# Optimization experiments

Hardware: AMD Instinct MI355X
Metric: run time of the kernel (lower is better)

## Reference

```python
import jax, jax.numpy as jnp
import numpy as np

H = W = 128      # image_shape
B = 64           # batch_size
O = 32           # orbit_size
RADIANS = True   # args.radians
RADIAN_INIT = 1.57
AFFINE_INIT = 0.1


def setup_inputs() -> dict:
    key = jax.random.key(0)
    k1, k2 = jax.random.split(key)
    X = jax.random.normal(k1, (B, H * W), dtype=jnp.float32)
    eps = jax.random.uniform(k2, (O, 7), dtype=jnp.float32)
    base = np.array([3.14, 1.0, 1.0, 1.0, 1.0, 1.0, 1.0], np.float32)
    ident = np.array([RADIAN_INIT, 1.0, 1.0, 0.0, 0.0, 0.0, 0.0], np.float32)
    tmin = ident - AFFINE_INIT * base
    tmax = np.array([-RADIAN_INIT, 1.0, 1.0, 0.0, 0.0, 0.0, 0.0], np.float32) + AFFINE_INIT * base
    return {
        "X": X,
        "eps": eps,
        "theta_min": jnp.asarray(tmin)[None, :],
        "theta_max": jnp.asarray(tmax)[None, :],
    }


def _affine_entries(thetas):
    # thetas: [O, 7] = [angle, sx, sy, shear_x, shear_y, tx, ty]
    # A = R(angle) @ [[sx, px], [py, sy]]  (rotation * scale/shear), t = [tx, ty]
    ang, sx, sy, px, py, tx, ty = (thetas[:, i] for i in range(7))
    if not RADIANS:
        ang = ang * (np.pi / 180.0)
    c, s = jnp.cos(ang), jnp.sin(ang)
    a00 = c * sx - s * py
    a01 = c * px - s * sy
    a10 = s * sx + c * py
    a11 = s * px + c * sy
    return a00, a01, a10, a11, tx, ty


def reference(X, eps, theta_min, theta_max):
    # sample orbit thetas: [O, 7]
    thetas = theta_min + (theta_max - theta_min) * eps
    a00, a01, a10, a11, tx, ty = _affine_entries(thetas)

    imgs = X.reshape(-1, H, W)  # [B, H, W]

    # normalized sampling grid in [-1, 1]
    xg = jnp.linspace(-1.0, 1.0, W, dtype=X.dtype)
    yg = jnp.linspace(-1.0, 1.0, H, dtype=X.dtype)
    Yg, Xg = jnp.meshgrid(yg, xg, indexing="ij")  # [H, W]

    # affine-transformed source coords per orbit sample: [O, H, W]
    xs = a00[:, None, None] * Xg + a01[:, None, None] * Yg + tx[:, None, None]
    ys = a10[:, None, None] * Xg + a11[:, None, None] * Yg + ty[:, None, None]

    # to pixel coords (align-corners convention)
    x = (xs + 1.0) * (W - 1) * 0.5
    y = (ys + 1.0) * (H - 1) * 0.5

    x0f = jnp.floor(x)
    y0f = jnp.floor(y)
    wx = x - x0f
    wy = y - y0f
    x0 = jnp.clip(x0f.astype(jnp.int32), 0, W - 1)
    x1 = jnp.clip(x0f.astype(jnp.int32) + 1, 0, W - 1)
    y0 = jnp.clip(y0f.astype(jnp.int32), 0, H - 1)
    y1 = jnp.clip(y0f.astype(jnp.int32) + 1, 0, H - 1)

    # gather 4 corners: fancy index over all images at once -> [B, O, H, W]
    Ia = imgs[:, y0, x0]
    Ib = imgs[:, y1, x0]
    Ic = imgs[:, y0, x1]
    Id = imgs[:, y1, x1]

    wa = (1.0 - wx) * (1.0 - wy)
    wb = (1.0 - wx) * wy
    wc = wx * (1.0 - wy)
    wd = wx * wy

    out = Ia * wa + Ib * wb + Ic * wc + Id * wd  # [B, O, H, W]
    out = jnp.transpose(out, (1, 0, 2, 3))       # [O, B, H, W]: per-theta batches
    return out.reshape(B * O, H, W, 1)
```

## Files before the change

kernel.cpp:

```cpp
#include <hip/hip_runtime.h>

#define HH 128
#define WW 128
#define BB 64
#define OO 32
#define LP 132

__launch_bounds__(1024, 8)
__global__ void sample_kernel(const float* __restrict__ X,
                              const float* __restrict__ eps,
                              const float* __restrict__ tmin,
                              const float* __restrict__ tmax,
                              float* __restrict__ out) {
    __shared__ float img[HH * LP];
    __shared__ float scoef[4][6];

    const int bid = blockIdx.x;
    const int og  = bid & 7;
    const int b   = bid >> 3;
    const int tid = threadIdx.x;

    if (tid < 4) {
        const int o = og * 4 + tid;
        float th[7];
#pragma unroll
        for (int i = 0; i < 7; ++i) {
            const float mn = tmin[i], mx = tmax[i];
            th[i] = mn + (mx - mn) * eps[o * 7 + i];
        }
        const float ang = th[0], sx = th[1], sy = th[2], px = th[3],
                    py = th[4], tx = th[5], ty = th[6];
        const float c = cosf(ang), s = sinf(ang);
        const float half = 0.5f * (WW - 1);
        scoef[tid][0] = (c * sx - s * py) * half;
        scoef[tid][1] = (c * px - s * sy) * half;
        scoef[tid][2] = (tx + 1.0f) * half;
        scoef[tid][3] = (s * sx + c * py) * half;
        scoef[tid][4] = (s * px + c * sy) * half;
        scoef[tid][5] = (ty + 1.0f) * half;
    }

    {
        const float4* __restrict__ src = (const float4*)(X + b * (HH * WW));
        float4* __restrict__ dst = (float4*)img;
#pragma unroll
        for (int i = 0; i < 4; ++i) {
            const int g = tid + i * 1024;
            dst[g + (g >> 5)] = src[g];
        }
    }
    __syncthreads();

    const int w  = tid & (WW - 1);
    const int h0 = tid >> 7;
    const float step  = 2.0f / 127.0f;
    const float hstep = 8.0f * step;
    const float Xg  = -1.0f + w * step;
    const float Yg0 = -1.0f + h0 * step;
    const float hi  = 126.999992f;

#pragma unroll
    for (int j = 0; j < 4; ++j) {
        const int o = og * 4 + j;
        const float cx0 = scoef[j][0];
        const float cx1 = scoef[j][1];
        const float cxt = scoef[j][2];
        const float cy0 = scoef[j][3];
        const float cy1 = scoef[j][4];
        const float cyt = scoef[j][5];

        float x = fmaf(cx1, Yg0, fmaf(cx0, Xg, cxt));
        float y = fmaf(cy1, Yg0, fmaf(cy0, Xg, cyt));
        const float dx = cx1 * hstep;
        const float dy = cy1 * hstep;

        float* __restrict__ outp =
            out + ((size_t)(o * BB + b) * (HH * WW)) + h0 * WW + w;

#pragma unroll
        for (int i = 0; i < 16; ++i) {
            const float xc = __builtin_amdgcn_fmed3f(x, 0.0f, hi);
            const float yc = __builtin_amdgcn_fmed3f(y, 0.0f, hi);
            const float x0f = floorf(xc);
            const float y0f = floorf(yc);
            const float wx = xc - x0f;
            const float wy = yc - y0f;
            const int idx = (int)fmaf(y0f, (float)LP, x0f);

            const float Ia = img[idx];
            const float Ic = img[idx + 1];
            const float Ib = img[idx + LP];
            const float Id = img[idx + LP + 1];

            const float top = fmaf(wx, Ic - Ia, Ia);
            const float bot = fmaf(wx, Id - Ib, Ib);
            *outp = fmaf(wy, bot - top, top);

            outp += 8 * WW;
            x += dx;
            y += dy;
        }
    }
}

extern "C" void kernel_launch(void* const* d_in, const int* in_sizes, int n_in,
                              void* d_out, int out_size, void* d_ws, size_t ws_size,
                              hipStream_t stream) {
    const float* X    = (const float*)d_in[0];
    const float* eps  = (const float*)d_in[1];
    const float* tmin = (const float*)d_in[2];
    const float* tmax = (const float*)d_in[3];
    float* out = (float*)d_out;

    const int nblocks = BB * 8;
    sample_kernel<<<nblocks, 1024, 0, stream>>>(X, eps, tmin, tmax, out);
}
```

Before: 150.0 us.

## Interleave vertically adjacent pixels in LDS as float2 to halve gather loads

Stores each source row paired with the row below as float2 entries in shared memory. The bilinear gather then needs two 64-bit LDS reads instead of four 32-bit reads. The layout doubles the per-pixel footprint (127x130 float2, about 132KB), so launch_bounds minimum blocks drops from 8 to 4 and the inner loop unroll is reduced to 8. Higher LDS use may cut occupancy, and 64-bit random accesses can raise bank conflicts.

Measured after the change: 150.0 us. Within noise of the previous version (-0.0%).

```diff
diff --git a/kernel.cpp b/kernel.cpp
--- a/kernel.cpp
+++ b/kernel.cpp
@@ -4,15 +4,15 @@
 #define WW 128
 #define BB 64
 #define OO 32
-#define LP 132
+#define LP2 130
 
-__launch_bounds__(1024, 8)
+__launch_bounds__(1024, 4)
 __global__ void sample_kernel(const float* __restrict__ X,
                               const float* __restrict__ eps,
                               const float* __restrict__ tmin,
                               const float* __restrict__ tmax,
                               float* __restrict__ out) {
-    __shared__ float img[HH * LP];
+    __shared__ float2 img2[127 * LP2];
     __shared__ float scoef[4][6];
 
     const int bid = blockIdx.x;
@@ -41,12 +41,21 @@
     }
 
     {
-        const float4* __restrict__ src = (const float4*)(X + b * (HH * WW));
-        float4* __restrict__ dst = (float4*)img;
+        const float4* __restrict__ src4 = (const float4*)(X + b * (HH * WW));
 #pragma unroll
         for (int i = 0; i < 4; ++i) {
             const int g = tid + i * 1024;
-            dst[g + (g >> 5)] = src[g];
+            if (g < 127 * 32) {
+                const int y  = g >> 5;
+                const int x4 = g & 31;
+                const float4 a = src4[(y << 5) + x4];
+                const float4 c = src4[(y << 5) + 32 + x4];
+                float2* __restrict__ d = &img2[y * LP2 + (x4 << 2)];
+                d[0] = make_float2(a.x, c.x);
+                d[1] = make_float2(a.y, c.y);
+                d[2] = make_float2(a.z, c.z);
+                d[3] = make_float2(a.w, c.w);
+            }
         }
     }
     __syncthreads();
@@ -77,7 +86,7 @@
         float* __restrict__ outp =
             out + ((size_t)(o * BB + b) * (HH * WW)) + h0 * WW + w;
 
-#pragma unroll
+#pragma unroll 8
         for (int i = 0; i < 16; ++i) {
             const float xc = __builtin_amdgcn_fmed3f(x, 0.0f, hi);
             const float yc = __builtin_amdgcn_fmed3f(y, 0.0f, hi);
@@ -85,15 +94,12 @@
             const float y0f = floorf(yc);
             const float wx = xc - x0f;
             const float wy = yc - y0f;
-            const int idx = (int)fmaf(y0f, (float)LP, x0f);
+            const int idx = (int)fmaf(y0f, (float)LP2, x0f);
 
-            const float Ia = img[idx];
-            const float Ic = img[idx + 1];
-            const float Ib = img[idx + LP];
-            const float Id = img[idx + LP + 1];
-
-            const float top = fmaf(wx, Ic - Ia, Ia);
-            const float bot = fmaf(wx, Id - Ib, Ib);
+            const float2 p0 = img2[idx];
+            const float2 p1 = img2[idx + 1];
+            const float top = fmaf(wx, p1.x - p0.x, p0.x);
+            const float bot = fmaf(wx, p1.y - p0.y, p0.y);
             *outp = fmaf(wy, bot - top, top);
 
             outp += 8 * WW;
```

## Compute two adjacent pixels per thread with 8-byte nontemporal stores

Applied to the files above, without the earlier changes.

Remaps threads so each computes two horizontally adjacent output pixels and writes them as one 8-byte vector store, using nontemporal stores to avoid cache pollution for the large write-only output. The row step doubles to 16 and the inner loop is unrolled by 4 instead of fully. Launch bounds min-blocks hint changes from 8 to 4, loosening register pressure. Fewer, wider stores aim to cut store instruction count in this write-bandwidth-bound kernel, at the cost of more live registers per thread.

Result: slower. 159.4 us (+6.3%).

```diff
diff --git a/kernel.cpp b/kernel.cpp
--- a/kernel.cpp
+++ b/kernel.cpp
@@ -6,7 +6,9 @@
 #define OO 32
 #define LP 132
 
-__launch_bounds__(1024, 8)
+typedef float f32x2 __attribute__((ext_vector_type(2)));
+
+__launch_bounds__(1024, 4)
 __global__ void sample_kernel(const float* __restrict__ X,
                               const float* __restrict__ eps,
                               const float* __restrict__ tmin,
@@ -51,11 +53,11 @@
     }
     __syncthreads();
 
-    const int w  = tid & (WW - 1);
-    const int h0 = tid >> 7;
+    const int x2 = (tid & 63) << 1;
+    const int h0 = tid >> 6;
     const float step  = 2.0f / 127.0f;
-    const float hstep = 8.0f * step;
-    const float Xg  = -1.0f + w * step;
+    const float rstep = 16.0f * step;
+    const float Xg0 = -1.0f + x2 * step;
     const float Yg0 = -1.0f + h0 * step;
     const float hi  = 126.999992f;
 
@@ -69,36 +71,49 @@
         const float cy1 = scoef[j][4];
         const float cyt = scoef[j][5];
 
-        float x = fmaf(cx1, Yg0, fmaf(cx0, Xg, cxt));
-        float y = fmaf(cy1, Yg0, fmaf(cy0, Xg, cyt));
-        const float dx = cx1 * hstep;
-        const float dy = cy1 * hstep;
+        const float ax = cx0 * step;
+        const float ay = cy0 * step;
+        const float dxr = cx1 * rstep;
+        const float dyr = cy1 * rstep;
 
-        float* __restrict__ outp =
-            out + ((size_t)(o * BB + b) * (HH * WW)) + h0 * WW + w;
+        float x = fmaf(cx1, Yg0, fmaf(cx0, Xg0, cxt));
+        float y = fmaf(cy1, Yg0, fmaf(cy0, Xg0, cyt));
 
+        f32x2* __restrict__ outp = (f32x2*)(
+            out + ((size_t)(o * BB + b) << 14) + h0 * WW + x2);
+
+#pragma unroll 4
+        for (int i = 0; i < 8; ++i) {
+            float r[2];
+            const float xb = x + ax;
+            const float yb = y + ay;
 #pragma unroll
-        for (int i = 0; i < 16; ++i) {
-            const float xc = __builtin_amdgcn_fmed3f(x, 0.0f, hi);
-            const float yc = __builtin_amdgcn_fmed3f(y, 0.0f, hi);
-            const float x0f = floorf(xc);
-            const float y0f = floorf(yc);
-            const float wx = xc - x0f;
-            const float wy = yc - y0f;
-            const int idx = (int)fmaf(y0f, (float)LP, x0f);
+            for (int k = 0; k < 2; ++k) {
+                const float xs = k ? xb : x;
+                const float ys = k ? yb : y;
+                const float xc = __builtin_amdgcn_fmed3f(xs, 0.0f, hi);
+                const float yc = __builtin_amdgcn_fmed3f(ys, 0.0f, hi);
+                const float x0f = floorf(xc);
+                const float y0f = floorf(yc);
+                const float wx = xc - x0f;
+                const float wy = yc - y0f;
+                const int idx = (int)fmaf(y0f, (float)LP, x0f);
 
-            const float Ia = img[idx];
-            const float Ic = img[idx + 1];
-            const float Ib = img[idx + LP];
-            const float Id = img[idx + LP + 1];
+                const float Ia = img[idx];
+                const float Ic = img[idx + 1];
+                const float Ib = img[idx + LP];
+                const float Id = img[idx + LP + 1];
 
-            const float top = fmaf(wx, Ic - Ia, Ia);
-            const float bot = fmaf(wx, Id - Ib, Ib);
-            *outp = fmaf(wy, bot - top, top);
+                const float top = fmaf(wx, Ic - Ia, Ia);
+                const float bot = fmaf(wx, Id - Ib, Ib);
+                r[k] = fmaf(wy, bot - top, top);
+            }
+            f32x2 v; v.x = r[0]; v.y = r[1];
+            __builtin_nontemporal_store(v, outp);
 
-            outp += 8 * WW;
-            x += dx;
-            y += dy;
+            outp += 16 * WW / 2;
+            x += dxr;
+            y += dyr;
         }
     }
 }
```
